# Performance work log

Hardware: AMD Instinct MI355X
Metric: run time of the kernel (lower is better)

Reference implementation:

```python
import jax, jax.numpy as jnp
import numpy as np

B, L, D = 2, 2048, 4096
H, KV, HD = 32, 8, 128          # query heads, kv heads, head_dim
G = H // KV                      # GQA group size
THETA = 10000.0
SCALE = HD ** -0.5


def apply_rope(x, offset=0):
    """Non-traditional (half-split) RoPE. x: [B, heads, L, HD]."""
    hd = x.shape[-1]
    half = hd // 2
    inv_freq = 1.0 / (THETA ** (jnp.arange(0, hd, 2, dtype=jnp.float32) / hd))  # [half]
    pos = jnp.arange(offset, offset + x.shape[2], dtype=jnp.float32)            # [L]
    ang = pos[:, None] * inv_freq[None, :]                                      # [L, half]
    cos = jnp.cos(ang).astype(x.dtype)
    sin = jnp.sin(ang).astype(x.dtype)
    x1, x2 = x[..., :half], x[..., half:]
    return jnp.concatenate([x1 * cos - x2 * sin, x2 * cos + x1 * sin], axis=-1)


def setup_inputs() -> dict:
    key = jax.random.key(0)
    ks = jax.random.split(key, 8)
    s = 0.02
    return {
        "x": jax.random.normal(ks[0], (B, L, D), dtype=jnp.float32),
        "Wq": jax.random.normal(ks[1], (D, H * HD), dtype=jnp.float32) * s,
        "bq": jnp.zeros((H * HD,), dtype=jnp.float32),
        "Wk": jax.random.normal(ks[2], (D, KV * HD), dtype=jnp.float32) * s,
        "bk": jnp.zeros((KV * HD,), dtype=jnp.float32),
        "Wv": jax.random.normal(ks[3], (D, KV * HD), dtype=jnp.float32) * s,
        "bv": jnp.zeros((KV * HD,), dtype=jnp.float32),
        "Wo": jax.random.normal(ks[4], (H * HD, D), dtype=jnp.float32) * s,
    }


def reference(x, Wq, bq, Wk, bk, Wv, bv, Wo):
    b, l, _ = x.shape
    # projections
    q = (x @ Wq + bq).reshape(b, l, H, HD).transpose(0, 2, 1, 3)   # [B,H,L,HD]
    k = (x @ Wk + bk).reshape(b, l, KV, HD).transpose(0, 2, 1, 3)  # [B,KV,L,HD]
    v = (x @ Wv + bv).reshape(b, l, KV, HD).transpose(0, 2, 1, 3)  # [B,KV,L,HD]
    # RoPE (cache=None path, offset 0)
    q = apply_rope(q)
    k = apply_rope(k)
    # GQA SDPA without materializing repeated KV heads
    qg = q.reshape(b, KV, G, l, HD)                                 # [B,KV,G,L,HD]
    scores = jnp.einsum('bkgld,bkmd->bkglm', qg, k) * SCALE         # [B,KV,G,L,L]
    probs = jax.nn.softmax(scores, axis=-1)
    out = jnp.einsum('bkglm,bkmd->bkgld', probs, v)                 # [B,KV,G,L,HD]
    out = out.reshape(b, H, l, HD).transpose(0, 2, 1, 3).reshape(b, l, H * HD)
    return out @ Wo
```

## Files before the change

kernel.cpp:

```cpp
#include <hip/hip_runtime.h>
#include <stdint.h>
#include <stddef.h>


typedef _Float16 half_t;
typedef __attribute__((ext_vector_type(4))) _Float16 f16x4;
typedef __attribute__((ext_vector_type(8))) _Float16 f16x8;
typedef __attribute__((ext_vector_type(4))) float f32x4;

#define NB 2
#define NL 2048
#define ND 4096
#define NH 32
#define NKV 8
#define NHD 128
#define NG 4
#define NQKV 6144
#define QK_SCALE 0.08838834764831845f
#define RLOG2E 1.4426950408889634f
#define M0 6.0f
#define THR 8.0f

static __device__ __forceinline__ void gll16(const void* g, void* l) {
  __builtin_amdgcn_global_load_lds(
      (__attribute__((address_space(1))) void*)(void*)(g),
      (__attribute__((address_space(3))) void*)(l),
      16, 0, 0);
}

__global__ void convert_f32_f16_kernel(const float* __restrict__ in,
                                       half_t* __restrict__ out, int n4) {
  int i = blockIdx.x * 256 + threadIdx.x;
  if (i >= n4) return;
  const float4 v = reinterpret_cast<const float4*>(in)[i];
  f16x4 o;
  o[0] = (half_t)v.x; o[1] = (half_t)v.y; o[2] = (half_t)v.z; o[3] = (half_t)v.w;
  reinterpret_cast<f16x4*>(out)[i] = o;
}

__global__ void wtrans_kernel(const float* __restrict__ W,
                              half_t* __restrict__ Wt, int K, int N) {
  __shared__ float tile[32][33];
  const int n0 = blockIdx.x * 32;
  const int k0 = blockIdx.y * 32;
  const int tx = threadIdx.x, ty = threadIdx.y;
#pragma unroll
  for (int r = 0; r < 32; r += 8)
    tile[ty + r][tx] = W[(size_t)(k0 + ty + r) * N + n0 + tx];
  __syncthreads();
#pragma unroll
  for (int r = 0; r < 32; r += 8)
    Wt[(size_t)(n0 + ty + r) * K + k0 + tx] = (half_t)tile[tx][ty + r];
}

template <typename OutT>
__global__ __launch_bounds__(256) void gemm_bt_kernel(
    const half_t* __restrict__ A, const half_t* __restrict__ Bt,
    const float* __restrict__ B0, const float* __restrict__ B1,
    const float* __restrict__ B2, OutT* __restrict__ C,
    int M, int N, int K) {
  constexpr int BK = 64;
  __shared__ half_t As[128 * BK];
  __shared__ half_t Bs[128 * BK];

  const int tid  = threadIdx.x;
  const int wave = tid >> 6;
  const int lane = tid & 63;
  const int r16  = lane & 15;
  const int quad = lane >> 4;
  const int wr = wave >> 1, wc = wave & 1;

  const int brow = blockIdx.y * 128;
  const int bcol = blockIdx.x * 128;

  const int rseg = lane >> 3;
  const int k8   = lane & 7;

  f32x4 acc[4][4] = {};

  for (int k0 = 0; k0 < K; k0 += BK) {
#pragma unroll
    for (int s = 0; s < 4; ++s) {
      const int seg = s * 4 + wave;
      const int row = seg * 8 + rseg;
      gll16(A  + (size_t)(brow + row) * K + k0 + k8 * 8, As + seg * 512);
      gll16(Bt + (size_t)(bcol + row) * K + k0 + k8 * 8, Bs + seg * 512);
    }
    asm volatile("s_waitcnt vmcnt(0)" ::: "memory");
    __syncthreads();

#pragma unroll
    for (int kc = 0; kc < 2; ++kc) {
      f16x8 af[4], bf[4];
#pragma unroll
      for (int mi = 0; mi < 4; ++mi)
        af[mi] = *reinterpret_cast<const f16x8*>(
            &As[(wr * 64 + mi * 16 + r16) * BK + kc * 32 + quad * 8]);
#pragma unroll
      for (int ni = 0; ni < 4; ++ni)
        bf[ni] = *reinterpret_cast<const f16x8*>(
            &Bs[(wc * 64 + ni * 16 + r16) * BK + kc * 32 + quad * 8]);
#pragma unroll
      for (int mi = 0; mi < 4; ++mi)
#pragma unroll
        for (int ni = 0; ni < 4; ++ni)
          acc[mi][ni] = __builtin_amdgcn_mfma_f32_16x16x32_f16(
              af[mi], bf[ni], acc[mi][ni], 0, 0, 0);
    }
    __syncthreads();
  }

#pragma unroll
  for (int ni = 0; ni < 4; ++ni) {
    const int col = bcol + wc * 64 + ni * 16 + r16;
    float bv = 0.0f;
    if (B0) bv = (col < ND) ? B0[col]
                            : (col < ND + NKV * NHD ? B1[col - ND]
                                                    : B2[col - ND - NKV * NHD]);
#pragma unroll
    for (int mi = 0; mi < 4; ++mi) {
      const int row0 = brow + wr * 64 + mi * 16 + quad * 4;
#pragma unroll
      for (int i = 0; i < 4; ++i)
        C[(size_t)(row0 + i) * N + col] = (OutT)(acc[mi][ni][i] + bv);
    }
  }
}

__global__ void ropepack_kernel(const half_t* __restrict__ rawh,
                                half_t* __restrict__ qb,
                                half_t* __restrict__ kb) {
  const size_t idx = (size_t)blockIdx.x * 256 + threadIdx.x;
  const int d = (int)(idx & 63);
  size_t t = idx >> 6;
  const int hp = (int)(t % (NH + NKV)); t /= (NH + NKV);
  const int l = (int)(t % NL);
  const int b = (int)(t / NL);
  const bool isQ = hp < NH;
  const int col0 = isQ ? hp * NHD : ND + (hp - NH) * NHD;
  const half_t* src = rawh + ((size_t)b * NL + l) * NQKV + col0;
  const float x1 = (float)src[d];
  const float x2 = (float)src[d + 64];
  const float inv_freq = exp2f(-(float)d * 0.20762050593045935f);
  const float ang = (float)l * inv_freq;
  float sn, cs;
  __sincosf(ang, &sn, &cs);
  const float scale = isQ ? QK_SCALE : 1.0f;
  half_t* dst = isQ ? qb + ((size_t)(b * NH + hp) * NL + l) * NHD
                    : kb + ((size_t)(b * NKV + (hp - NH)) * NL + l) * NHD;
  dst[d]      = (half_t)((x1 * cs - x2 * sn) * scale);
  dst[d + 64] = (half_t)((x2 * cs + x1 * sn) * scale);
}

__global__ void vtrans16_kernel(const half_t* __restrict__ rawh,
                                half_t* __restrict__ Vt) {
  __shared__ half_t tile[32][34];
  const int bkv = blockIdx.z;
  const int l0 = blockIdx.x * 32;
  const int d0 = blockIdx.y * 32;
  const int b = bkv / NKV, kvh = bkv % NKV;
  const int tx = threadIdx.x, ty = threadIdx.y;
#pragma unroll
  for (int r = 0; r < 32; r += 8)
    tile[ty + r][tx] = rawh[(size_t)(b * NL + l0 + ty + r) * NQKV
                            + ND + NKV * NHD + kvh * NHD + d0 + tx];
  __syncthreads();
  half_t* dst = Vt + (size_t)bkv * NHD * NL;
#pragma unroll
  for (int r = 0; r < 32; r += 8)
    dst[(size_t)(d0 + ty + r) * NL + l0 + tx] = tile[tx][ty + r];
}

#define KVB 64

__global__ __launch_bounds__(512, 2) void attn_kernel(
    const half_t* __restrict__ Q,
    const half_t* __restrict__ Kh,
    const half_t* __restrict__ Vt,
    half_t* __restrict__ O) {
  __shared__ half_t Ks[2][KVB * NHD];
  __shared__ half_t Vs[2][NHD * KVB];
  __shared__ half_t Ps[8][16 * 64];

  const int tid = threadIdx.x;
  const int wave = tid >> 6, lane = tid & 63;
  const int r16 = lane & 15, quad = lane >> 4;
  const int r7 = r16 & 7;

  const int bid = (int)blockIdx.x;
  const int swz = (bid & 7) * 64 + (bid >> 3);
  const int nqt = NL / 256;
  const int bh = swz / nqt, qt = swz % nqt;
  const int b = bh / NH, h = bh % NH;
  const int kvh = h / NG;

  const int qrow0 = qt * 256 + wave * 32;
  const half_t* Qb = Q  + ((size_t)(b * NH + h) * NL + qrow0) * NHD;
  const half_t* Kb = Kh + ((size_t)(b * NKV + kvh) * NL) * NHD;
  const half_t* Vb = Vt + ((size_t)(b * NKV + kvh) * NHD) * NL;
  half_t* Pw = &Ps[wave][0];

  auto stage = [&](int buf, int n0) {
#pragma unroll
    for (int j = 0; j < 2; ++j) {
      const int slot = j * 512 + wave * 64 + lane;
      {
        const int row = slot >> 4;
        const int c = (slot & 15) ^ (row & 7);
        gll16(Kb + (size_t)(n0 + row) * NHD + c * 8,
              &Ks[buf][(j * 512 + wave * 64) * 8]);
      }
      {
        const int row = slot >> 3;
        const int c = (slot & 7) ^ (row & 7);
        gll16(Vb + (size_t)row * NL + n0 + c * 8,
              &Vs[buf][(j * 512 + wave * 64) * 8]);
      }
    }
  };

  stage(0, 0);

  f16x8 qf[2][4];
#pragma unroll
  for (int rt = 0; rt < 2; ++rt)
#pragma unroll
    for (int c = 0; c < 4; ++c)
      qf[rt][c] = *reinterpret_cast<const f16x8*>(
          &Qb[(size_t)(rt * 16 + r16) * NHD + c * 32 + quad * 8]);

  f32x4 oacc[2][8];
  float m_run[2][4], lsum[2][4];
#pragma unroll
  for (int rt = 0; rt < 2; ++rt) {
#pragma unroll
    for (int i = 0; i < 4; ++i) { m_run[rt][i] = M0; lsum[rt][i] = 0.0f; }
#pragma unroll
    for (int dt = 0; dt < 8; ++dt) oacc[rt][dt] = (f32x4){0.f, 0.f, 0.f, 0.f};
  }

  const int swzread = r7 ^ ((r16 >> 3) * 5);

  asm volatile("s_waitcnt vmcnt(0)" ::: "memory");
  __syncthreads();

  int cur = 0;
  for (int t = 0; t < NL / KVB; ++t, cur ^= 1) {
    if (t + 1 < NL / KVB) stage(cur ^ 1, (t + 1) * KVB);

    const half_t* Kc = &Ks[cur][0];
    const half_t* Vc = &Vs[cur][0];

    f32x4 s[2][4] = {};
#pragma unroll
    for (int c = 0; c < 4; ++c) {
      const int ch = ((c * 4 + quad) ^ r7) * 8;
#pragma unroll
      for (int nt = 0; nt < 4; ++nt) {
        f16x8 kf = *reinterpret_cast<const f16x8*>(&Kc[(nt * 16 + r16) * NHD + ch]);
        s[0][nt] = __builtin_amdgcn_mfma_f32_16x16x32_f16(qf[0][c], kf, s[0][nt], 0, 0, 0);
        s[1][nt] = __builtin_amdgcn_mfma_f32_16x16x32_f16(qf[1][c], kf, s[1][nt], 0, 0, 0);
      }
    }

    float mx[2][4];
    bool need = false;
#pragma unroll
    for (int rt = 0; rt < 2; ++rt)
#pragma unroll
      for (int i = 0; i < 4; ++i) {
        mx[rt][i] = fmaxf(fmaxf(s[rt][0][i], s[rt][1][i]),
                          fmaxf(s[rt][2][i], s[rt][3][i]));
        need = need || (mx[rt][i] > m_run[rt][i] + THR);
      }
    if (__any(need ? 1 : 0)) {
#pragma unroll
      for (int rt = 0; rt < 2; ++rt)
#pragma unroll
        for (int i = 0; i < 4; ++i) {
          float m = mx[rt][i];
#pragma unroll
          for (int off = 1; off < 16; off <<= 1)
            m = fmaxf(m, __shfl_xor(m, off));
          const float mn = fmaxf(m_run[rt][i], m);
          const float corr = exp2f((m_run[rt][i] - mn) * RLOG2E);
          m_run[rt][i] = mn;
          lsum[rt][i] *= corr;
#pragma unroll
          for (int dt = 0; dt < 8; ++dt) oacc[rt][dt][i] *= corr;
        }
    }

    f16x8 pa[2][2];
#pragma unroll
    for (int rt = 0; rt < 2; ++rt) {
#pragma unroll
      for (int i = 0; i < 4; ++i) {
        const float mrl = m_run[rt][i] * RLOG2E;
        float p[4];
#pragma unroll
        for (int nt = 0; nt < 4; ++nt)
          p[nt] = exp2f(s[rt][nt][i] * RLOG2E - mrl);
        lsum[rt][i] += (p[0] + p[1]) + (p[2] + p[3]);
        const int row = quad * 4 + i;
        const int swzr = (row & 7) ^ ((row >> 3) * 5);
#pragma unroll
        for (int nt = 0; nt < 4; ++nt)
          Pw[row * 64 + (((nt * 2 + (r16 >> 3)) ^ swzr) * 8) + r7] = (half_t)p[nt];
      }
      pa[rt][0] = *reinterpret_cast<const f16x8*>(&Pw[r16 * 64 + ((quad ^ swzread) * 8)]);
      pa[rt][1] = *reinterpret_cast<const f16x8*>(&Pw[r16 * 64 + (((4 + quad) ^ swzread) * 8)]);
    }

    const int ch0 = (quad ^ r7) * 8;
    const int ch1 = ((4 + quad) ^ r7) * 8;
#pragma unroll
    for (int dt = 0; dt < 8; ++dt) {
      const int row = dt * 16 + r16;
      f16x8 v0 = *reinterpret_cast<const f16x8*>(&Vc[row * 64 + ch0]);
      f16x8 v1 = *reinterpret_cast<const f16x8*>(&Vc[row * 64 + ch1]);
      oacc[0][dt] = __builtin_amdgcn_mfma_f32_16x16x32_f16(pa[0][0], v0, oacc[0][dt], 0, 0, 0);
      oacc[0][dt] = __builtin_amdgcn_mfma_f32_16x16x32_f16(pa[0][1], v1, oacc[0][dt], 0, 0, 0);
      oacc[1][dt] = __builtin_amdgcn_mfma_f32_16x16x32_f16(pa[1][0], v0, oacc[1][dt], 0, 0, 0);
      oacc[1][dt] = __builtin_amdgcn_mfma_f32_16x16x32_f16(pa[1][1], v1, oacc[1][dt], 0, 0, 0);
    }

    asm volatile("s_waitcnt vmcnt(0)" ::: "memory");
    __syncthreads();
  }

  half_t* Ob = O + ((size_t)(b * NL) + qrow0) * (NH * NHD) + (size_t)h * NHD;
#pragma unroll
  for (int rt = 0; rt < 2; ++rt)
#pragma unroll
    for (int i = 0; i < 4; ++i) {
      float l = lsum[rt][i];
#pragma unroll
      for (int off = 1; off < 16; off <<= 1)
        l += __shfl_xor(l, off);
      const float inv = 1.0f / l;
      const int rl = rt * 16 + quad * 4 + i;
#pragma unroll
      for (int dt = 0; dt < 8; ++dt)
        Ob[(size_t)rl * (NH * NHD) + dt * 16 + r16] =
            (half_t)(oacc[rt][dt][i] * inv);
    }
}

extern "C" void kernel_launch(void* const* d_in, const int* in_sizes, int n_in,
                              void* d_out, int out_size, void* d_ws, size_t ws_size,
                              hipStream_t stream) {
  const float* x  = (const float*)d_in[0];
  const float* Wq = (const float*)d_in[1];
  const float* bq = (const float*)d_in[2];
  const float* Wk = (const float*)d_in[3];
  const float* bk = (const float*)d_in[4];
  const float* Wv = (const float*)d_in[5];
  const float* bv = (const float*)d_in[6];
  const float* Wo = (const float*)d_in[7];
  float* out = (float*)d_out;

  char* ws = (char*)d_ws;
  size_t off = 0;
  auto alloc = [&](size_t bytes) {
    size_t cur = off;
    off += (bytes + 255) & ~(size_t)255;
    return cur;
  };
  const size_t M = (size_t)NB * NL;
  half_t* xb   = (half_t*)(ws + alloc(M * ND * 2));
  half_t* wqkv = (half_t*)(ws + alloc((size_t)NQKV * ND * 2));
  half_t* rawh = (half_t*)(ws + alloc(M * NQKV * 2));
  half_t* qb   = (half_t*)(ws + alloc(M * (size_t)(NH * NHD) * 2));
  half_t* kb   = (half_t*)(ws + alloc(M * (size_t)(NKV * NHD) * 2));
  half_t* vt   = (half_t*)(ws + alloc(M * (size_t)(NKV * NHD) * 2));

  {
    int n4 = (int)(M * ND / 4);
    convert_f32_f16_kernel<<<dim3((n4 + 255) / 256), dim3(256), 0, stream>>>(x, xb, n4);
  }
  wtrans_kernel<<<dim3(ND / 32, ND / 32), dim3(32, 8), 0, stream>>>(
      Wq, wqkv, ND, ND);
  wtrans_kernel<<<dim3((NKV * NHD) / 32, ND / 32), dim3(32, 8), 0, stream>>>(
      Wk, wqkv + (size_t)ND * ND, ND, NKV * NHD);
  wtrans_kernel<<<dim3((NKV * NHD) / 32, ND / 32), dim3(32, 8), 0, stream>>>(
      Wv, wqkv + (size_t)(ND + NKV * NHD) * ND, ND, NKV * NHD);

  gemm_bt_kernel<half_t><<<dim3(NQKV / 128, M / 128), dim3(256), 0, stream>>>(
      xb, wqkv, bq, bk, bv, rawh, (int)M, NQKV, ND);

  ropepack_kernel<<<dim3((unsigned)(M * (NH + NKV) * 64 / 256)), dim3(256), 0, stream>>>(
      rawh, qb, kb);
  vtrans16_kernel<<<dim3(NL / 32, NHD / 32, NB * NKV), dim3(32, 8), 0, stream>>>(rawh, vt);

  wtrans_kernel<<<dim3(ND / 32, ND / 32), dim3(32, 8), 0, stream>>>(Wo, wqkv, NH * NHD, ND);

  attn_kernel<<<dim3(NB * NH * (NL / 256)), dim3(512), 0, stream>>>(qb, kb, vt, xb);

  gemm_bt_kernel<float><<<dim3(ND / 128, M / 128), dim3(256), 0, stream>>>(
      xb, wqkv, nullptr, nullptr, nullptr, out, (int)M, ND, ND);
}
```

Before: 761.8 us.

## Replace GEMM with 256x256-tile, 4-stage pipelined, swizzled-LDS kernel

```diff
diff --git a/kernel.cpp b/kernel.cpp
--- a/kernel.cpp
+++ b/kernel.cpp
@@ -54,72 +54,99 @@
 }
 
 template <typename OutT>
-__global__ __launch_bounds__(256) void gemm_bt_kernel(
+__global__ __launch_bounds__(512, 2) void gemm256_kernel(
     const half_t* __restrict__ A, const half_t* __restrict__ Bt,
     const float* __restrict__ B0, const float* __restrict__ B1,
     const float* __restrict__ B2, OutT* __restrict__ C,
     int M, int N, int K) {
-  constexpr int BK = 64;
-  __shared__ half_t As[128 * BK];
-  __shared__ half_t Bs[128 * BK];
-
-  const int tid  = threadIdx.x;
-  const int wave = tid >> 6;
-  const int lane = tid & 63;
-  const int r16  = lane & 15;
-  const int quad = lane >> 4;
-  const int wr = wave >> 1, wc = wave & 1;
-
-  const int brow = blockIdx.y * 128;
-  const int bcol = blockIdx.x * 128;
-
-  const int rseg = lane >> 3;
-  const int k8   = lane & 7;
-
-  f32x4 acc[4][4] = {};
-
-  for (int k0 = 0; k0 < K; k0 += BK) {
-#pragma unroll
-    for (int s = 0; s < 4; ++s) {
-      const int seg = s * 4 + wave;
-      const int row = seg * 8 + rseg;
-      gll16(A  + (size_t)(brow + row) * K + k0 + k8 * 8, As + seg * 512);
-      gll16(Bt + (size_t)(bcol + row) * K + k0 + k8 * 8, Bs + seg * 512);
-    }
-    asm volatile("s_waitcnt vmcnt(0)" ::: "memory");
-    __syncthreads();
-
-#pragma unroll
-    for (int kc = 0; kc < 2; ++kc) {
-      f16x8 af[4], bf[4];
-#pragma unroll
-      for (int mi = 0; mi < 4; ++mi)
-        af[mi] = *reinterpret_cast<const f16x8*>(
-            &As[(wr * 64 + mi * 16 + r16) * BK + kc * 32 + quad * 8]);
+  constexpr int BK = 32;
+  __shared__ __align__(16) half_t As[4][256 * BK];
+  __shared__ __align__(16) half_t Bs[4][256 * BK];
+
+  const int tid = threadIdx.x;
+  const int wave = tid >> 6, lane = tid & 63;
+  const int r16 = lane & 15, quad = lane >> 4;
+  const int wm = wave >> 2, wn = wave & 3;
+
+  const int nbx = N >> 8;
+  const int lid = (int)(blockIdx.y * gridDim.x + blockIdx.x);
+  const int nwg = (int)(gridDim.x * gridDim.y);
+  const int cpx = nwg >> 3;
+  const int swz = (lid & 7) * cpx + (lid >> 3);
+  const int brow = (swz / nbx) * 256;
+  const int bcol = (swz % nbx) * 256;
+
+  const int NT = K >> 5;
+
+  auto stage = [&](int t) {
+    const int buf = t & 3;
+    const int k0 = t << 5;
+#pragma unroll
+    for (int j = 0; j < 2; ++j) {
+      const int s = j * 512 + wave * 64 + lane;
+      const int row = s >> 2;
+      const int cg = (s & 3) ^ (row & 3);
+      gll16(A  + (size_t)(brow + row) * K + k0 + cg * 8,
+            &As[buf][(j * 512 + wave * 64) * 8]);
+      gll16(Bt + (size_t)(bcol + row) * K + k0 + cg * 8,
+            &Bs[buf][(j * 512 + wave * 64) * 8]);
+    }
+  };
+
+  f32x4 acc[8][4] = {};
+
+  stage(0); stage(1); stage(2);
+  asm volatile("s_waitcnt vmcnt(8)" ::: "memory");
+  __builtin_amdgcn_s_barrier();
+
+  for (int t = 0; t < NT; ++t) {
+    if (t > 0) {
+      asm volatile("s_waitcnt lgkmcnt(0)" ::: "memory");
+      __builtin_amdgcn_s_barrier();
+    }
+    if (t + 3 < NT) {
+      stage(t + 3);
+      asm volatile("s_waitcnt vmcnt(8)" ::: "memory");
+    } else if (t + 2 < NT) {
+      asm volatile("s_waitcnt vmcnt(4)" ::: "memory");
+    } else if (t + 1 < NT) {
+      asm volatile("s_waitcnt vmcnt(0)" ::: "memory");
+    }
+
+    const int buf = t & 3;
+    const half_t* Ab = &As[buf][0];
+    const half_t* Bb = &Bs[buf][0];
+    const int csw = (quad ^ (r16 & 3)) << 3;
+
+    f16x8 bf[4];
+#pragma unroll
+    for (int ni = 0; ni < 4; ++ni) {
+      const int col = wn * 64 + ni * 16 + r16;
+      bf[ni] = *reinterpret_cast<const f16x8*>(&Bb[col * BK + csw]);
+    }
+    __builtin_amdgcn_s_setprio(1);
+#pragma unroll
+    for (int mi = 0; mi < 8; ++mi) {
+      const int row = wm * 128 + mi * 16 + r16;
+      const f16x8 af = *reinterpret_cast<const f16x8*>(&Ab[row * BK + csw]);
 #pragma unroll
       for (int ni = 0; ni < 4; ++ni)
-        bf[ni] = *reinterpret_cast<const f16x8*>(
-            &Bs[(wc * 64 + ni * 16 + r16) * BK + kc * 32 + quad * 8]);
-#pragma unroll
-      for (int mi = 0; mi < 4; ++mi)
-#pragma unroll
-        for (int ni = 0; ni < 4; ++ni)
-          acc[mi][ni] = __builtin_amdgcn_mfma_f32_16x16x32_f16(
-              af[mi], bf[ni], acc[mi][ni], 0, 0, 0);
-    }
-    __syncthreads();
+        acc[mi][ni] = __builtin_amdgcn_mfma_f32_16x16x32_f16(
+            af, bf[ni], acc[mi][ni], 0, 0, 0);
+    }
+    __builtin_amdgcn_s_setprio(0);
   }
 
 #pragma unroll
   for (int ni = 0; ni < 4; ++ni) {
-    const int col = bcol + wc * 64 + ni * 16 + r16;
+    const int col = bcol + wn * 64 + ni * 16 + r16;
     float bv = 0.0f;
     if (B0) bv = (col < ND) ? B0[col]
                             : (col < ND + NKV * NHD ? B1[col - ND]
                                                     : B2[col - ND - NKV * NHD]);
 #pragma unroll
-    for (int mi = 0; mi < 4; ++mi) {
-      const int row0 = brow + wr * 64 + mi * 16 + quad * 4;
+    for (int mi = 0; mi < 8; ++mi) {
+      const int row0 = brow + wm * 128 + mi * 16 + quad * 4;
 #pragma unroll
       for (int i = 0; i < 4; ++i)
         C[(size_t)(row0 + i) * N + col] = (OutT)(acc[mi][ni][i] + bv);
@@ -386,7 +413,7 @@
   wtrans_kernel<<<dim3((NKV * NHD) / 32, ND / 32), dim3(32, 8), 0, stream>>>(
       Wv, wqkv + (size_t)(ND + NKV * NHD) * ND, ND, NKV * NHD);
 
-  gemm_bt_kernel<half_t><<<dim3(NQKV / 128, M / 128), dim3(256), 0, stream>>>(
+  gemm256_kernel<half_t><<<dim3(NQKV / 256, M / 256), dim3(512), 0, stream>>>(
       xb, wqkv, bq, bk, bv, rawh, (int)M, NQKV, ND);
 
   ropepack_kernel<<<dim3((unsigned)(M * (NH + NKV) * 64 / 256)), dim3(256), 0, stream>>>(
@@ -397,6 +424,6 @@
 
   attn_kernel<<<dim3(NB * NH * (NL / 256)), dim3(512), 0, stream>>>(qb, kb, vt, xb);
 
-  gemm_bt_kernel<float><<<dim3(ND / 128, M / 128), dim3(256), 0, stream>>>(
+  gemm256_kernel<float><<<dim3(ND / 256, M / 256), dim3(512), 0, stream>>>(
       xb, wqkv, nullptr, nullptr, nullptr, out, (int)M, ND, ND);
 }
```

New measurement: 775.4 us. About the same (+1.8%).
